# Optimization experiments

Measured on AMD Instinct MI355X. Metric: run time of the kernel, lower is better.

## Reference

```python
import jax, jax.numpy as jnp
import numpy as np

N_NODES = 10000
N_EDGES = 160000
IN_DIM = 256
HID = 128
HEADS = 8
OUT_DIM = 64
LN_EPS = 1e-5
NEG_SLOPE = 0.2


def _gat_layer(x, W, att_src, att_dst, bias, src, dst, heads, out_ch, n):
    # x: [N, F_in]; W: [F_in, heads*out_ch]; att_*: [heads, out_ch]; bias: [heads*out_ch]
    xl = (x @ W).reshape(n, heads, out_ch)              # [N, H, C]
    a_src = jnp.einsum('nhc,hc->nh', xl, att_src)        # [N, H]
    a_dst = jnp.einsum('nhc,hc->nh', xl, att_dst)        # [N, H]
    e = a_src[src] + a_dst[dst]                          # [E, H]
    e = jnp.where(e > 0, e, NEG_SLOPE * e)               # leaky_relu(0.2)
    e_max = jax.ops.segment_max(e, dst, num_segments=n)  # segment softmax (stable)
    e = jnp.exp(e - e_max[dst])
    denom = jax.ops.segment_sum(e, dst, num_segments=n)
    alpha = e / (denom[dst] + 1e-16)                     # [E, H]
    msg = xl[src] * alpha[:, :, None]                    # [E, H, C]
    out = jax.ops.segment_sum(msg, dst, num_segments=n)  # [N, H, C]
    return out.reshape(n, heads * out_ch) + bias


def setup_inputs() -> dict:
    key = jax.random.key(0)
    ks = jax.random.split(key, 12)
    s = 0.05
    inp = {
        'x': jax.random.normal(ks[0], (N_NODES, IN_DIM), dtype=jnp.float32),
        'edge_index': jax.random.randint(ks[1], (2, N_EDGES), 0, N_NODES, dtype=jnp.int32),
        'W1': jax.random.normal(ks[2], (IN_DIM, HEADS * HID), dtype=jnp.float32) * s,
        'att_src1': jax.random.normal(ks[3], (HEADS, HID), dtype=jnp.float32) * s,
        'att_dst1': jax.random.normal(ks[4], (HEADS, HID), dtype=jnp.float32) * s,
        'b1': jnp.zeros((HEADS * HID,), dtype=jnp.float32),
        'W2': jax.random.normal(ks[5], (HEADS * HID, OUT_DIM), dtype=jnp.float32) * s,
        'att_src2': jax.random.normal(ks[6], (1, OUT_DIM), dtype=jnp.float32) * s,
        'att_dst2': jax.random.normal(ks[7], (1, OUT_DIM), dtype=jnp.float32) * s,
        'b2': jnp.zeros((OUT_DIM,), dtype=jnp.float32),
        'gamma': jnp.ones((OUT_DIM,), dtype=jnp.float32),
        'beta': jnp.zeros((OUT_DIM,), dtype=jnp.float32),
    }
    return inp


def reference(x, edge_index, W1, att_src1, att_dst1, b1, W2, att_src2, att_dst2, b2, gamma, beta):
    n = x.shape[0]
    # GATConv adds self-loops by default
    loops = jnp.arange(n, dtype=edge_index.dtype)
    src = jnp.concatenate([edge_index[0], loops])
    dst = jnp.concatenate([edge_index[1], loops])
    h = _gat_layer(x, W1, att_src1, att_dst1, b1, src, dst, HEADS, HID, n)
    h = jax.nn.elu(h)  # dropout is identity in eval mode
    h = _gat_layer(h, W2, att_src2, att_dst2, b2, src, dst, 1, OUT_DIM, n)
    mu = jnp.mean(h, axis=-1, keepdims=True)
    var = jnp.mean(jnp.square(h - mu), axis=-1, keepdims=True)
    return (h - mu) / jnp.sqrt(var + LN_EPS) * gamma + beta
```

## Files before the change

kernel.cpp:

```cpp
#include <hip/hip_runtime.h>

#define N_NODES 10000
#define N_EDGES 160000
#define E_TOT   (N_EDGES + N_NODES)
#define IN_DIM  256
#define HID     128
#define HEADS   8
#define F1      (HEADS*HID)
#define OUT_DIM 64
#define CAP     64
#define LN_EPS  1e-5f
#define NEG_SLOPE 0.2f

typedef __attribute__((ext_vector_type(8))) short short8;
typedef __attribute__((ext_vector_type(4))) float f32x4;

static __device__ __forceinline__ float lrelu(float e){ return e > 0.f ? e : NEG_SLOPE*e; }

static __device__ __forceinline__ ushort f2bf(float f){
  union { float f; uint32_t u; } v; v.f = f;
  uint32_t u = v.u;
  return (ushort)((u + 0x7FFFu + ((u >> 16) & 1u)) >> 16);
}
static __device__ __forceinline__ float bf2f(ushort h){
  union { uint32_t u; float f; } v; v.u = ((uint32_t)h) << 16; return v.f;
}
#define BLO(u) bf2f((ushort)((u) & 0xffffu))
#define BHI(u) bf2f((ushort)((u) >> 16))


__global__ __launch_bounds__(256) void k_prologue(const float* __restrict__ x, ushort* __restrict__ xb,
                          const float* __restrict__ W1, ushort* __restrict__ W1T,
                          const float* __restrict__ W2, ushort* __restrict__ W2T,
                          const float* __restrict__ att_s1, const float* __restrict__ att_d1,
                          float* __restrict__ w_as, float* __restrict__ w_ad,
                          int* __restrict__ counts){
  __shared__ float tile[64][65];
  const int NB_CVT = (N_NODES*IN_DIM/4)/256;
  int bid = blockIdx.x;
  if (bid < NB_CVT){
    int i = bid*256 + threadIdx.x;
    float4 v = *(const float4*)&x[(size_t)i*4];
    uint2 o;
    o.x = (uint32_t)f2bf(v.x) | ((uint32_t)f2bf(v.y) << 16);
    o.y = (uint32_t)f2bf(v.z) | ((uint32_t)f2bf(v.w) << 16);
    *(uint2*)&xb[(size_t)i*4] = o;
    return;
  }
  bid -= NB_CVT;
  if (bid < 80){
    const float* W; ushort* WT; int R, C, rt, ct;
    if (bid < 64){ W = W1; WT = W1T; R = IN_DIM; C = F1; rt = bid & 3; ct = bid >> 2; }
    else         { W = W2; WT = W2T; R = F1; C = OUT_DIM; rt = bid - 64; ct = 0; }
    int r0 = rt*64, c0 = ct*64;
    int t = threadIdx.x;
    int sub = t >> 4, q4 = (t & 15)*4;
    #pragma unroll
    for (int p = 0; p < 4; p++){
      int r = sub + p*16;
      float4 v = *(const float4*)&W[(size_t)(r0 + r)*C + c0 + q4];
      tile[r][q4]   = v.x; tile[r][q4+1] = v.y;
      tile[r][q4+2] = v.z; tile[r][q4+3] = v.w;
    }
    __syncthreads();
    #pragma unroll
    for (int p = 0; p < 4; p++){
      int c = sub + p*16;
      uint2 o;
      o.x = (uint32_t)f2bf(tile[q4+0][c]) | ((uint32_t)f2bf(tile[q4+1][c]) << 16);
      o.y = (uint32_t)f2bf(tile[q4+2][c]) | ((uint32_t)f2bf(tile[q4+3][c]) << 16);
      *(uint2*)&WT[(size_t)(c0 + c)*R + r0 + q4] = o;
    }
    return;
  }
  bid -= 80;
  if (bid < 512){
    int wg = bid*4 + (threadIdx.x >> 6);
    int lane = threadIdx.x & 63;
    int h = wg >> 8, i = wg & 255;
    if (h >= HEADS) return;
    int c = lane*2;
    float2 wv = *(const float2*)&W1[(size_t)i*F1 + h*HID + c];
    float2 as = *(const float2*)&att_s1[h*HID + c];
    float2 ad = *(const float2*)&att_d1[h*HID + c];
    float s = wv.x*as.x + wv.y*as.y;
    float d = wv.x*ad.x + wv.y*ad.y;
    #pragma unroll
    for (int o = 32; o > 0; o >>= 1){ s += __shfl_xor(s, o); d += __shfl_xor(d, o); }
    if (lane == 0){ w_as[h*IN_DIM + i] = s; w_ad[h*IN_DIM + i] = d; }
    return;
  }
  bid -= 512;
  int i = bid*256 + threadIdx.x;
  if (i < N_NODES) counts[i] = 0;
}


__global__ __launch_bounds__(256) void k_phase2(const int* __restrict__ ei,
                          int* __restrict__ cnt, int* __restrict__ pcsr,
                          const ushort* __restrict__ xb,
                          const float* __restrict__ w_as, const float* __restrict__ w_ad,
                          float* __restrict__ as1, float* __restrict__ ad1){
  const int NB_SC = (E_TOT + 255)/256;
  int bid = blockIdx.x;
  if (bid < NB_SC){
    int e = bid*256 + threadIdx.x;
    if (e >= E_TOT) return;
    int src, dst;
    if (e < N_EDGES){ src = ei[e]; dst = ei[N_EDGES + e]; }
    else            { src = e - N_EDGES; dst = src; }
    int pos = atomicAdd(&cnt[dst], 1);
    if (pos < CAP) pcsr[dst*CAP + pos] = src;
    return;
  }
  bid -= NB_SC;
  int n = bid*4 + (threadIdx.x >> 6);
  int lane = threadIdx.x & 63;
  if (n >= N_NODES) return;
  int c0 = lane*4;
  uint2 px = *(const uint2*)&xb[(size_t)n*IN_DIM + c0];
  float x0 = BLO(px.x), x1 = BHI(px.x), x2 = BLO(px.y), x3 = BHI(px.y);
  float s[HEADS], d[HEADS];
  #pragma unroll
  for (int h = 0; h < HEADS; h++){
    float4 ws = *(const float4*)&w_as[h*IN_DIM + c0];
    float4 wd = *(const float4*)&w_ad[h*IN_DIM + c0];
    s[h] = x0*ws.x + x1*ws.y + x2*ws.z + x3*ws.w;
    d[h] = x0*wd.x + x1*wd.y + x2*wd.z + x3*wd.w;
  }
  #pragma unroll
  for (int o = 32; o > 0; o >>= 1){
    #pragma unroll
    for (int h = 0; h < HEADS; h++){ s[h] += __shfl_xor(s[h], o); d[h] += __shfl_xor(d[h], o); }
  }
  if (lane == 0){
    #pragma unroll
    for (int h = 0; h < HEADS; h++){ as1[n*HEADS + h] = s[h]; ad1[n*HEADS + h] = d[h]; }
  }
}


__global__ __launch_bounds__(256) void k_aggpre(const ushort* __restrict__ xb,
                       const float* __restrict__ a_src, const float* __restrict__ a_dst,
                       const int* __restrict__ counts, const int* __restrict__ pcsr,
                       ushort* __restrict__ h1pre){
  __shared__ ushort xs[32][IN_DIM + 8];
  __shared__ float  als[CAP][HEADS];
  __shared__ int    ssl[CAP];
  int n = blockIdx.x;
  int k = counts[n]; if (k > CAP) k = CAP;
  int base = n*CAP;
  int t = threadIdx.x;

  if (t < 64){
    int lane = t;
    bool act = lane < k;
    int s = act ? pcsr[base + lane] : 0;
    ssl[lane] = s;
    float4 ad0 = *(const float4*)&a_dst[n*HEADS];
    float4 ad1v = *(const float4*)&a_dst[n*HEADS + 4];
    float e[HEADS];
    if (act){
      float4 v0 = *(const float4*)&a_src[s*HEADS];
      float4 v1 = *(const float4*)&a_src[s*HEADS + 4];
      e[0] = lrelu(v0.x + ad0.x); e[1] = lrelu(v0.y + ad0.y);
      e[2] = lrelu(v0.z + ad0.z); e[3] = lrelu(v0.w + ad0.w);
      e[4] = lrelu(v1.x + ad1v.x); e[5] = lrelu(v1.y + ad1v.y);
      e[6] = lrelu(v1.z + ad1v.z); e[7] = lrelu(v1.w + ad1v.w);
    } else {
      #pragma unroll
      for (int h = 0; h < HEADS; h++) e[h] = -1e30f;
    }
    float lm[HEADS];
    #pragma unroll
    for (int h = 0; h < HEADS; h++) lm[h] = e[h];
    #pragma unroll
    for (int o = 32; o > 0; o >>= 1){
      #pragma unroll
      for (int h = 0; h < HEADS; h++) lm[h] = fmaxf(lm[h], __shfl_xor(lm[h], o));
    }
    float wv[HEADS], ls[HEADS];
    #pragma unroll
    for (int h = 0; h < HEADS; h++){
      wv[h] = act ? __expf(e[h] - lm[h]) : 0.f;
      ls[h] = wv[h];
    }
    #pragma unroll
    for (int o = 32; o > 0; o >>= 1){
      #pragma unroll
      for (int h = 0; h < HEADS; h++) ls[h] += __shfl_xor(ls[h], o);
    }
    #pragma unroll
    for (int h = 0; h < HEADS; h++) als[lane][h] = wv[h]/(ls[h] + 1e-16f);
  }
  __syncthreads();

  int er = t >> 3, ec = t & 7;
  int g = t >> 5, c = t & 31;
  float a[8];
  #pragma unroll
  for (int j = 0; j < 8; j++) a[j] = 0.f;

  for (int i0 = 0; i0 < k; i0 += 32){
    int ne = k - i0; if (ne > 32) ne = 32;
    if (er < ne){
      const ushort* p = &xb[(size_t)ssl[i0 + er]*IN_DIM + ec*32];
      uint4 r0 = *(const uint4*)p;
      uint4 r1 = *(const uint4*)(p + 8);
      uint4 r2 = *(const uint4*)(p + 16);
      uint4 r3 = *(const uint4*)(p + 24);
      *(uint4*)&xs[er][ec*32]      = r0;
      *(uint4*)&xs[er][ec*32 + 8]  = r1;
      *(uint4*)&xs[er][ec*32 + 16] = r2;
      *(uint4*)&xs[er][ec*32 + 24] = r3;
    }
    __syncthreads();
    for (int e = 0; e < ne; e++){
      float w = als[i0 + e][g];
      uint4 p = *(const uint4*)&xs[e][c*8];
      a[0] += w*BLO(p.x); a[1] += w*BHI(p.x);
      a[2] += w*BLO(p.y); a[3] += w*BHI(p.y);
      a[4] += w*BLO(p.z); a[5] += w*BHI(p.z);
      a[6] += w*BLO(p.w); a[7] += w*BHI(p.w);
    }
    __syncthreads();
  }
  uint4 o;
  o.x = (uint32_t)f2bf(a[0]) | ((uint32_t)f2bf(a[1]) << 16);
  o.y = (uint32_t)f2bf(a[2]) | ((uint32_t)f2bf(a[3]) << 16);
  o.z = (uint32_t)f2bf(a[4]) | ((uint32_t)f2bf(a[5]) << 16);
  o.w = (uint32_t)f2bf(a[6]) | ((uint32_t)f2bf(a[7]) << 16);
  *(uint4*)&h1pre[(size_t)n*(HEADS*IN_DIM) + g*IN_DIM + c*8] = o;
}


template<int BM, int BN, int WAVES_N, int WM, int WN, int OUT_MODE, bool FUSE_ATT, int AHS>
__global__ __launch_bounds__(256) void k_gemm_bf16(const ushort* __restrict__ A,
                                                   const ushort* __restrict__ Bt,
                                                   void* __restrict__ Cout,
                                                   const float* __restrict__ bias,
                                                   const float* __restrict__ att_s,
                                                   const float* __restrict__ att_d,
                                                   float* __restrict__ out_as,
                                                   float* __restrict__ out_ad,
                                                   int M, int N, int K, int lda){
  const int LDK = 40;
  __shared__ ushort As[BM][LDK];
  __shared__ ushort Bs[BN][LDK];
  int tid = threadIdx.x;
  int lane = tid & 63, wid = tid >> 6;
  int wm = wid / WAVES_N, wn = wid % WAVES_N;
  int row0 = blockIdx.x * BM, col0 = blockIdx.y * BN;
  int aoff = blockIdx.y * AHS;
  int wrow = wm * (WM*16), wcol = wn * (WN*16);

  f32x4 acc[WM][WN];
  #pragma unroll
  for (int i = 0; i < WM; i++)
    #pragma unroll
    for (int j = 0; j < WN; j++)
      acc[i][j] = (f32x4){0.f, 0.f, 0.f, 0.f};

  int koff = (lane >> 4) * 8;
  int frow = lane & 15;
  int g = tid & 3, r = tid >> 2;

  for (int k0 = 0; k0 < K; k0 += 32){
    #pragma unroll
    for (int it = 0; it < BM/64; it++){
      int rr = r + it*64;
      int grow = row0 + rr;
      short8 v = (short8){0,0,0,0,0,0,0,0};
      if (grow < M) v = *(const short8*)&A[(size_t)grow*lda + aoff + k0 + g*8];
      *(short8*)&As[rr][g*8] = v;
    }
    #pragma unroll
    for (int it = 0; it < BN/64; it++){
      int rr = r + it*64;
      short8 v = *(const short8*)&Bt[(size_t)(col0 + rr)*K + k0 + g*8];
      *(short8*)&Bs[rr][g*8] = v;
    }
    __syncthreads();
    short8 af[WM], bf[WN];
    #pragma unroll
    for (int i = 0; i < WM; i++) af[i] = *(short8*)&As[wrow + i*16 + frow][koff];
    #pragma unroll
    for (int j = 0; j < WN; j++) bf[j] = *(short8*)&Bs[wcol + j*16 + frow][koff];
    #pragma unroll
    for (int i = 0; i < WM; i++)
      #pragma unroll
      for (int j = 0; j < WN; j++)
        acc[i][j] = __builtin_amdgcn_mfma_f32_16x16x32_bf16(af[i], bf[j], acc[i][j], 0, 0, 0);
    __syncthreads();
  }

  int lr = (lane >> 4) * 4, lc = lane & 15;

  #pragma unroll
  for (int i = 0; i < WM; i++){
    #pragma unroll
    for (int j = 0; j < WN; j++){
      int gc = col0 + wcol + j*16 + lc;
      #pragma unroll
      for (int q = 0; q < 4; q++){
        int gr = row0 + wrow + i*16 + lr + q;
        if (gr < M){
          if (OUT_MODE == 0){
            ((float*)Cout)[(size_t)gr*N + gc] = acc[i][j][q];
          } else if (OUT_MODE == 1){
            ((ushort*)Cout)[(size_t)gr*N + gc] = f2bf(acc[i][j][q]);
          } else {
            float v = acc[i][j][q] + bias[gc];
            v = v > 0.f ? v : __expf(v) - 1.f;
            ((ushort*)Cout)[(size_t)gr*N + gc] = f2bf(v);
          }
        }
      }
    }
  }

  if (FUSE_ATT){
    __shared__ float red_s[BM], red_d[BM];
    int head = blockIdx.y;
    int NH = gridDim.y;
    float asw[WN], adw[WN];
    #pragma unroll
    for (int j = 0; j < WN; j++){
      int c2 = wcol + j*16 + lc;
      asw[j] = att_s[head*BN + c2];
      adw[j] = att_d[head*BN + c2];
    }
    float ps[WM][4], pd[WM][4];
    #pragma unroll
    for (int i = 0; i < WM; i++){
      #pragma unroll
      for (int q = 0; q < 4; q++){
        float s = 0.f, d = 0.f;
        #pragma unroll
        for (int j = 0; j < WN; j++){ s += acc[i][j][q]*asw[j]; d += acc[i][j][q]*adw[j]; }
        #pragma unroll
        for (int o = 8; o > 0; o >>= 1){ s += __shfl_xor(s, o); d += __shfl_xor(d, o); }
        ps[i][q] = s; pd[i][q] = d;
      }
    }
    if (WAVES_N == 2){
      if (wn == 1 && lc == 0){
        #pragma unroll
        for (int i = 0; i < WM; i++)
          #pragma unroll
          for (int q = 0; q < 4; q++){
            red_s[wrow + i*16 + lr + q] = ps[i][q];
            red_d[wrow + i*16 + lr + q] = pd[i][q];
          }
      }
      __syncthreads();
      if (wn == 0 && lc == 0){
        #pragma unroll
        for (int i = 0; i < WM; i++)
          #pragma unroll
          for (int q = 0; q < 4; q++){
            ps[i][q] += red_s[wrow + i*16 + lr + q];
            pd[i][q] += red_d[wrow + i*16 + lr + q];
          }
      }
    }
    if (lc == 0 && (WAVES_N == 1 || wn == 0)){
      #pragma unroll
      for (int i = 0; i < WM; i++)
        #pragma unroll
        for (int q = 0; q < 4; q++){
          int gr = row0 + wrow + i*16 + lr + q;
          if (gr < M){
            out_as[(size_t)gr*NH + head] = ps[i][q];
            out_ad[(size_t)gr*NH + head] = pd[i][q];
          }
        }
    }
  }
}


__global__ __launch_bounds__(256) void k_agg2(const float* __restrict__ xl,
                       const float* __restrict__ a_src, const float* __restrict__ a_dst,
                       const int* __restrict__ counts, const int* __restrict__ pcsr,
                       const float* __restrict__ b2,
                       const float* __restrict__ gamma, const float* __restrict__ beta,
                       float* __restrict__ out){
  int n = blockIdx.x*4 + (threadIdx.x >> 6);
  int lane = threadIdx.x & 63;
  if (n >= N_NODES) return;
  int k = counts[n]; if (k > CAP) k = CAP;
  int base = n*CAP;
  float ad = a_dst[n];

  int sv = 0; float ev = -1e30f;
  if (lane < k){
    sv = pcsr[base + lane];
    ev = lrelu(a_src[sv] + ad);
  }
  float lm = ev;
  #pragma unroll
  for (int o = 32; o > 0; o >>= 1) lm = fmaxf(lm, __shfl_xor(lm, o));
  float wv = (lane < k) ? __expf(ev - lm) : 0.f;
  float ls = wv;
  #pragma unroll
  for (int o = 32; o > 0; o >>= 1) ls += __shfl_xor(ls, o);
  wv *= 1.f/(ls + 1e-16f);

  float acc0 = 0.f, acc1 = 0.f;
  int i = 0;
  for (; i + 1 < k; i += 2){
    int   s0 = __shfl(sv, i);     float w0 = __shfl(wv, i);
    int   s1 = __shfl(sv, i + 1); float w1 = __shfl(wv, i + 1);
    acc0 += w0*xl[(size_t)s0*OUT_DIM + lane];
    acc1 += w1*xl[(size_t)s1*OUT_DIM + lane];
  }
  if (i < k){
    int s0 = __shfl(sv, i); float w0 = __shfl(wv, i);
    acc0 += w0*xl[(size_t)s0*OUT_DIM + lane];
  }
  float v = acc0 + acc1 + b2[lane];

  float mu = v;
  #pragma unroll
  for (int o = 32; o > 0; o >>= 1) mu += __shfl_xor(mu, o);
  mu *= (1.f/OUT_DIM);
  float d = v - mu;
  float var = d*d;
  #pragma unroll
  for (int o = 32; o > 0; o >>= 1) var += __shfl_xor(var, o);
  var *= (1.f/OUT_DIM);
  out[(size_t)n*OUT_DIM + lane] = d*rsqrtf(var + LN_EPS)*gamma[lane] + beta[lane];
}


extern "C" void kernel_launch(void* const* d_in, const int* in_sizes, int n_in,
                              void* d_out, int out_size, void* d_ws, size_t ws_size,
                              hipStream_t stream){
  const float* x        = (const float*)d_in[0];
  const int*   ei       = (const int*)  d_in[1];
  const float* W1       = (const float*)d_in[2];
  const float* att_src1 = (const float*)d_in[3];
  const float* att_dst1 = (const float*)d_in[4];
  const float* b1       = (const float*)d_in[5];
  const float* W2       = (const float*)d_in[6];
  const float* att_src2 = (const float*)d_in[7];
  const float* att_dst2 = (const float*)d_in[8];
  const float* b2       = (const float*)d_in[9];
  const float* gamma    = (const float*)d_in[10];
  const float* beta     = (const float*)d_in[11];
  float* out = (float*)d_out;

  char* w = (char*)d_ws;
  auto carve = [&](size_t bytes)->void*{
    void* p = (void*)w; w += (bytes + 255) & ~(size_t)255; return p;
  };
  ushort* xb      = (ushort*)carve((size_t)N_NODES*IN_DIM*sizeof(ushort));
  ushort* W1T     = (ushort*)carve((size_t)F1*IN_DIM*sizeof(ushort));
  ushort* W2T     = (ushort*)carve((size_t)OUT_DIM*F1*sizeof(ushort));
  ushort* h1pre   = (ushort*)carve((size_t)N_NODES*HEADS*IN_DIM*sizeof(ushort));
  ushort* h1b     = (ushort*)carve((size_t)N_NODES*F1*sizeof(ushort));
  float*  xl2     = (float*) carve((size_t)N_NODES*OUT_DIM*sizeof(float));
  float*  w_as    = (float*) carve((size_t)HEADS*IN_DIM*sizeof(float));
  float*  w_ad    = (float*) carve((size_t)HEADS*IN_DIM*sizeof(float));
  float*  as1     = (float*) carve((size_t)N_NODES*HEADS*sizeof(float));
  float*  ad1     = (float*) carve((size_t)N_NODES*HEADS*sizeof(float));
  float*  as2     = (float*) carve((size_t)N_NODES*sizeof(float));
  float*  ad2     = (float*) carve((size_t)N_NODES*sizeof(float));
  int*    counts  = (int*)   carve((size_t)N_NODES*sizeof(int));
  int*    pcsr    = (int*)   carve((size_t)N_NODES*CAP*sizeof(int));

  const int NB4 = (N_NODES + 3)/4;
  const int MT128 = (N_NODES + 127)/128;
  const int MT64  = (N_NODES + 63)/64;
  const int NB_SC = (E_TOT + 255)/256;

  const int NB_PRO = (N_NODES*IN_DIM/4)/256 + 80 + 512 + 40;
  k_prologue<<<NB_PRO, 256, 0, stream>>>(x, xb, W1, W1T, W2, W2T,
                                         att_src1, att_dst1, w_as, w_ad, counts);
  k_phase2<<<NB_SC + NB4, 256, 0, stream>>>(ei, counts, pcsr, xb, w_as, w_ad, as1, ad1);
  k_aggpre<<<N_NODES, 256, 0, stream>>>(xb, as1, ad1, counts, pcsr, h1pre);
  k_gemm_bf16<128, 128, 2, 4, 4, 2, false, IN_DIM><<<dim3(MT128, HEADS), 256, 0, stream>>>(
      h1pre, W1T, h1b, b1, nullptr, nullptr, nullptr, nullptr,
      N_NODES, F1, IN_DIM, HEADS*IN_DIM);
  k_gemm_bf16<64, 64, 2, 2, 2, 0, true, 0><<<dim3(MT64, 1), 256, 0, stream>>>(
      h1b, W2T, xl2, nullptr, att_src2, att_dst2, as2, ad2,
      N_NODES, OUT_DIM, F1, F1);
  k_agg2<<<NB4, 256, 0, stream>>>(xl2, as2, ad2, counts, pcsr, b2, gamma, beta, out);
}
```

Baseline: 197.2 us.

## Prefetch neighbor feature rows into registers and overlap with softmax in aggpre

Result: slower. 201.5 us (+2.2%).

```diff
diff --git a/kernel.cpp b/kernel.cpp
--- a/kernel.cpp
+++ b/kernel.cpp
@@ -151,6 +151,20 @@
   int k = counts[n]; if (k > CAP) k = CAP;
   int base = n*CAP;
   int t = threadIdx.x;
+  int er = t >> 3, ec = t & 7;
+  int g = t >> 5, c = t & 31;
+
+  uint4 r0, r1, r2, r3;
+  {
+    int ne = k < 32 ? k : 32;
+    if (er < ne){
+      const ushort* p = &xb[(size_t)pcsr[base + er]*IN_DIM + ec*8];
+      r0 = *(const uint4*)p;
+      r1 = *(const uint4*)(p + 64);
+      r2 = *(const uint4*)(p + 128);
+      r3 = *(const uint4*)(p + 192);
+    }
+  }
 
   if (t < 64){
     int lane = t;
@@ -195,8 +209,6 @@
   }
   __syncthreads();
 
-  int er = t >> 3, ec = t & 7;
-  int g = t >> 5, c = t & 31;
   float a[8];
   #pragma unroll
   for (int j = 0; j < 8; j++) a[j] = 0.f;
@@ -204,24 +216,45 @@
   for (int i0 = 0; i0 < k; i0 += 32){
     int ne = k - i0; if (ne > 32) ne = 32;
     if (er < ne){
-      const ushort* p = &xb[(size_t)ssl[i0 + er]*IN_DIM + ec*32];
-      uint4 r0 = *(const uint4*)p;
-      uint4 r1 = *(const uint4*)(p + 8);
-      uint4 r2 = *(const uint4*)(p + 16);
-      uint4 r3 = *(const uint4*)(p + 24);
-      *(uint4*)&xs[er][ec*32]      = r0;
-      *(uint4*)&xs[er][ec*32 + 8]  = r1;
-      *(uint4*)&xs[er][ec*32 + 16] = r2;
-      *(uint4*)&xs[er][ec*32 + 24] = r3;
+      *(uint4*)&xs[er][ec*8]       = r0;
+      *(uint4*)&xs[er][ec*8 + 64]  = r1;
+      *(uint4*)&xs[er][ec*8 + 128] = r2;
+      *(uint4*)&xs[er][ec*8 + 192] = r3;
     }
     __syncthreads();
-    for (int e = 0; e < ne; e++){
-      float w = als[i0 + e][g];
-      uint4 p = *(const uint4*)&xs[e][c*8];
-      a[0] += w*BLO(p.x); a[1] += w*BHI(p.x);
-      a[2] += w*BLO(p.y); a[3] += w*BHI(p.y);
-      a[4] += w*BLO(p.z); a[5] += w*BHI(p.z);
-      a[6] += w*BLO(p.w); a[7] += w*BHI(p.w);
+    int i1 = i0 + 32;
+    if (i1 < k){
+      int ne2 = k - i1; if (ne2 > 32) ne2 = 32;
+      if (er < ne2){
+        const ushort* p = &xb[(size_t)ssl[i1 + er]*IN_DIM + ec*8];
+        r0 = *(const uint4*)p;
+        r1 = *(const uint4*)(p + 64);
+        r2 = *(const uint4*)(p + 128);
+        r3 = *(const uint4*)(p + 192);
+      }
+    }
+    int e = 0;
+    for (; e + 1 < ne; e += 2){
+      float wA = als[i0 + e][g];
+      float wB = als[i0 + e + 1][g];
+      uint4 pA = *(const uint4*)&xs[e][c*8];
+      uint4 pB = *(const uint4*)&xs[e + 1][c*8];
+      a[0] += wA*BLO(pA.x) + wB*BLO(pB.x);
+      a[1] += wA*BHI(pA.x) + wB*BHI(pB.x);
+      a[2] += wA*BLO(pA.y) + wB*BLO(pB.y);
+      a[3] += wA*BHI(pA.y) + wB*BHI(pB.y);
+      a[4] += wA*BLO(pA.z) + wB*BLO(pB.z);
+      a[5] += wA*BHI(pA.z) + wB*BHI(pB.z);
+      a[6] += wA*BLO(pA.w) + wB*BLO(pB.w);
+      a[7] += wA*BHI(pA.w) + wB*BHI(pB.w);
+    }
+    if (e < ne){
+      float wA = als[i0 + e][g];
+      uint4 pA = *(const uint4*)&xs[e][c*8];
+      a[0] += wA*BLO(pA.x); a[1] += wA*BHI(pA.x);
+      a[2] += wA*BLO(pA.y); a[3] += wA*BHI(pA.y);
+      a[4] += wA*BLO(pA.z); a[5] += wA*BHI(pA.z);
+      a[6] += wA*BLO(pA.w); a[7] += wA*BHI(pA.w);
     }
     __syncthreads();
   }
```
